# Performance work log

Measured on AMD Instinct MI355X. Metric: run time of the kernel, lower is better.

## Reference

```python
import jax, jax.numpy as jnp
import numpy as np

B, N, D = 32, 4096, 256
H, DH, S = 8, 64, 16
DI = H * DH          # dim_inner = 512
HID = 1024           # max(dim, hidden_dim)
ITERS = 3
EPS = 1e-8
SCALE = D ** (-0.5)  # NOTE: original uses dim, not dim_head


def _ln(x, g, b):
    m = jnp.mean(x, axis=-1, keepdims=True)
    v = jnp.mean((x - m) ** 2, axis=-1, keepdims=True)
    return (x - m) * jax.lax.rsqrt(v + 1e-5) * g + b


def _lin(x, W, b):  # torch layout: W [out, in]
    return x @ W.T + b


def setup_inputs() -> dict:
    key = jax.random.key(0)
    ks = jax.random.split(key, 32)

    def p(i, shape, s=0.02):
        return jax.random.normal(ks[i], shape, dtype=jnp.float32) * s

    return {
        "x": jax.random.normal(ks[0], (B, N, D), dtype=jnp.float32),
        "slots_noise": jax.random.normal(ks[1], (B, S, D), dtype=jnp.float32),
        "slots_mu": p(2, (1, 1, D), 1.0),
        "slots_logsigma": p(3, (1, 1, D)),
        "ln_in_g": jnp.ones((D,), jnp.float32), "ln_in_b": jnp.zeros((D,), jnp.float32),
        "ln_s_g": jnp.ones((D,), jnp.float32), "ln_s_b": jnp.zeros((D,), jnp.float32),
        "ln_ff_g": jnp.ones((D,), jnp.float32), "ln_ff_b": jnp.zeros((D,), jnp.float32),
        "Wq": p(4, (DI, D)), "bq": jnp.zeros((DI,), jnp.float32),
        "Wk": p(5, (DI, D)), "bk": jnp.zeros((DI,), jnp.float32),
        "Wv": p(6, (DI, D)), "bv": jnp.zeros((DI,), jnp.float32),
        "Wc": p(7, (D, DI)), "bc": jnp.zeros((D,), jnp.float32),
        "gru_wih": p(8, (3 * D, D)), "gru_whh": p(9, (3 * D, D)),
        "gru_bih": jnp.zeros((3 * D,), jnp.float32), "gru_bhh": jnp.zeros((3 * D,), jnp.float32),
        "W1": p(10, (HID, D)), "b1": jnp.zeros((HID,), jnp.float32),
        "W2": p(11, (D, HID)), "b2": jnp.zeros((D,), jnp.float32),
    }


def reference(x, slots_noise, slots_mu, slots_logsigma,
              ln_in_g, ln_in_b, ln_s_g, ln_s_b, ln_ff_g, ln_ff_b,
              Wq, bq, Wk, bk, Wv, bv, Wc, bc,
              gru_wih, gru_whh, gru_bih, gru_bhh,
              W1, b1, W2, b2):
    slots = slots_mu + jnp.exp(slots_logsigma) * slots_noise  # [B,S,D]
    xn = _ln(x, ln_in_g, ln_in_b)
    k = _lin(xn, Wk, bk).reshape(B, N, H, DH)  # [B,N,H,DH]
    v = _lin(xn, Wv, bv).reshape(B, N, H, DH)

    for _ in range(ITERS):
        slots_prev = slots
        sn = _ln(slots, ln_s_g, ln_s_b)
        q = _lin(sn, Wq, bq).reshape(B, S, H, DH)             # [B,S,H,DH]
        logits = jnp.einsum('bihd,bjhd->bhij', q, k) * SCALE  # [B,H,S,N]
        attn = jax.nn.softmax(logits, axis=-1) + EPS
        attn = attn / jnp.sum(attn, axis=-1, keepdims=True)
        upd = jnp.einsum('bhij,bjhd->bihd', attn, v).reshape(B, S, DI)
        upd = _lin(upd, Wc, bc)                               # [B,S,D]
        # GRUCell (torch gate order r, z, n)
        gi = _lin(upd.reshape(-1, D), gru_wih, gru_bih)
        gh = _lin(slots_prev.reshape(-1, D), gru_whh, gru_bhh)
        ir, iz, inn = jnp.split(gi, 3, axis=-1)
        hr, hz, hn = jnp.split(gh, 3, axis=-1)
        r = jax.nn.sigmoid(ir + hr)
        z = jax.nn.sigmoid(iz + hz)
        n = jnp.tanh(inn + r * hn)
        slots = ((1.0 - z) * n + z * slots_prev.reshape(-1, D)).reshape(B, S, D)
        slots = slots + _lin(jax.nn.relu(_lin(_ln(slots, ln_ff_g, ln_ff_b), W1, b1)), W2, b2)
    return slots
```

## Files before the change

### kernel.cpp

```cpp
#include <hip/hip_runtime.h>
#include <stdint.h>

#define B_   32
#define N_   4096
#define D_   256
#define H_   8
#define S_   16
#define DI_  512
#define HID_ 1024
#define CH_  8
#define NCHUNK_ 512
#define SCALE_ 0.0625f

typedef short  short8 __attribute__((ext_vector_type(8)));
typedef float  f32x4  __attribute__((ext_vector_type(4)));

__device__ __forceinline__ unsigned short f2bf(float x){
  union { float f; unsigned u; } v; v.f = x;
  unsigned r = v.u + 0x7FFFu + ((v.u >> 16) & 1u);
  return (unsigned short)(r >> 16);
}

#define FMA4(acc, a, Wm) do { (acc)[0] += (a)*(Wm).x; (acc)[1] += (a)*(Wm).y; (acc)[2] += (a)*(Wm).z; (acc)[3] += (a)*(Wm).w; } while(0)

__global__ void k_badws(float* out){ out[blockIdx.x*256 + threadIdx.x] = 1e9f; }

__global__ __launch_bounds__(256) void k_init_slots(
    const float* __restrict__ noise, const float* __restrict__ mu,
    const float* __restrict__ lsig, float* __restrict__ slots)
{
  int i = blockIdx.x*256 + threadIdx.x;
  int d = i & 255;
  slots[i] = mu[d] + expf(lsig[d]) * noise[i];
}

__global__ __launch_bounds__(256) void k_transpose(
    const float* __restrict__ src, float* __restrict__ dst, int R, int C)
{
  __shared__ float t[32][33];
  int c0 = blockIdx.x*32, r0 = blockIdx.y*32;
  int tx = threadIdx.x, ty = threadIdx.y;
  for (int j = 0; j < 32; j += 8){
    int r = r0 + ty + j, c = c0 + tx;
    if (r < R && c < C) t[ty+j][tx] = src[(size_t)r*C + c];
  }
  __syncthreads();
  for (int j = 0; j < 32; j += 8){
    int c = c0 + ty + j, r = r0 + tx;
    if (c < C && r < R) dst[(size_t)c*R + r] = t[tx][ty+j];
  }
}

__global__ __launch_bounds__(256) void k_ln_x(
    const float* __restrict__ x, const float* __restrict__ g, const float* __restrict__ bb,
    unsigned short* __restrict__ xn, unsigned short* __restrict__ xnT)
{
  __shared__ __align__(16) char tile[32768];
  const int blk = blockIdx.x;
  const int b  = blk >> 6;
  const int n0 = (blk & 63) * 64;
  const int t = threadIdx.x;
  const int lane = t & 63;
  const int w = t >> 6;
  float4 gv = *(const float4*)&g[lane*4];
  float4 bv = *(const float4*)&bb[lane*4];
#pragma unroll 1
  for (int it = 0; it < 16; ++it){
    const int nl = w*16 + it;
    const size_t row = (size_t)b*N_ + n0 + nl;
    float4 xv = *(const float4*)&x[row*256 + lane*4];
    float s = xv.x + xv.y + xv.z + xv.w;
    float q = xv.x*xv.x + xv.y*xv.y + xv.z*xv.z + xv.w*xv.w;
#pragma unroll
    for (int m = 1; m < 64; m <<= 1){ s += __shfl_xor(s, m); q += __shfl_xor(q, m); }
    float mean = s * 0.00390625f;
    float var  = q * 0.00390625f - mean*mean;
    float rs = rsqrtf(var + 1e-5f);
    unsigned short u0 = f2bf((xv.x-mean)*rs*gv.x + bv.x);
    unsigned short u1 = f2bf((xv.y-mean)*rs*gv.y + bv.y);
    unsigned short u2 = f2bf((xv.z-mean)*rs*gv.z + bv.z);
    unsigned short u3 = f2bf((xv.w-mean)*rs*gv.w + bv.w);
    uint2 pk; pk.x = (unsigned)u0 | ((unsigned)u1 << 16); pk.y = (unsigned)u2 | ((unsigned)u3 << 16);
    *(uint2*)&xn[row*256 + lane*4] = pk;
    *(uint2*)(tile + nl*512 + ((lane*8) ^ ((nl & 7) << 4))) = pk;
  }
  __syncthreads();
#pragma unroll 1
  for (int j = 0; j < 32; ++j){
    int flat = j*256 + t;
    int d  = flat >> 5;
    int np = (flat & 31) * 2;
    unsigned short lo = *(const unsigned short*)(tile + np*512     + ((2*d) ^ ((np     & 7) << 4)));
    unsigned short hi = *(const unsigned short*)(tile + (np+1)*512 + ((2*d) ^ (((np+1) & 7) << 4)));
    *(unsigned*)&xnT[((size_t)b*D_ + d)*N_ + n0 + np] = (unsigned)lo | ((unsigned)hi << 16);
  }
}

__global__ __launch_bounds__(256) void k_preA(
    const float* __restrict__ slots, const float* __restrict__ lsg, const float* __restrict__ lsb,
    const float* __restrict__ WqT, const float* __restrict__ bq, float* __restrict__ ql)
{
  __shared__ __align__(16) float a[4][256];
  const int lane = threadIdx.x & 63, w = threadIdx.x >> 6;
  const int row = blockIdx.x*4 + w;
  const int o   = blockIdx.y*64 + lane;
  float4 v = *(const float4*)&slots[(size_t)row*D_ + lane*4];
  float s = v.x + v.y + v.z + v.w;
  float q = v.x*v.x + v.y*v.y + v.z*v.z + v.w*v.w;
#pragma unroll
  for (int m = 1; m < 64; m <<= 1){ s += __shfl_xor(s, m); q += __shfl_xor(q, m); }
  float mean = s * 0.00390625f;
  float var  = q * 0.00390625f - mean*mean;
  float rs = rsqrtf(var + 1e-5f);
  float4 gv = *(const float4*)&lsg[lane*4];
  float4 bv = *(const float4*)&lsb[lane*4];
  a[w][lane*4+0] = (v.x-mean)*rs*gv.x + bv.x;
  a[w][lane*4+1] = (v.y-mean)*rs*gv.y + bv.y;
  a[w][lane*4+2] = (v.z-mean)*rs*gv.z + bv.z;
  a[w][lane*4+3] = (v.w-mean)*rs*gv.w + bv.w;
  const float* Wp = WqT + o;
  float acc = 0.f;
#pragma unroll 4
  for (int k4 = 0; k4 < 64; ++k4){
    float4 av = *(const float4*)&a[w][k4*4];
    acc += av.x * Wp[(size_t)(k4*4+0)*512];
    acc += av.y * Wp[(size_t)(k4*4+1)*512];
    acc += av.z * Wp[(size_t)(k4*4+2)*512];
    acc += av.w * Wp[(size_t)(k4*4+3)*512];
  }
  ql[(size_t)row*DI_ + o] = acc + bq[o];
}

__global__ __launch_bounds__(256) void k_preB(
    const float* __restrict__ ql, const float* __restrict__ Wk, const float* __restrict__ bk,
    unsigned short* __restrict__ qp, float* __restrict__ qb)
{
  __shared__ __align__(16) float qs[16][64];
  const int id = blockIdx.x;
  const int b  = id >> 3;
  const int h  = id & 7;
  const int cb = blockIdx.y;
  const int c0 = cb*64;
  const int t = threadIdx.x;
  const int lane = t & 63, w = t >> 6;
  {
    int flat = t*4;
    int s = flat >> 6, k = flat & 63;
    *(float4*)&qs[s][k] = *(const float4*)&ql[((size_t)(b*S_ + s))*DI_ + h*64 + k];
  }
  __syncthreads();
  if (cb == 0){
    float bkv = bk[h*64 + lane];
#pragma unroll
    for (int r = 0; r < 4; ++r){
      int s = w*4 + r;
      float v = qs[s][lane] * bkv;
#pragma unroll
      for (int m = 1; m < 64; m <<= 1) v += __shfl_xor(v, m);
      if (lane == 0) qb[((size_t)b*H_ + h)*S_ + s] = v * SCALE_;
    }
  }
  float acc[4] = {};
  const float* Wp = Wk + (size_t)(h*64)*256 + c0 + lane;
#pragma unroll 4
  for (int k = 0; k < 64; ++k){
    float wv = Wp[(size_t)k*256];
    acc[0] += qs[w*4+0][k] * wv;
    acc[1] += qs[w*4+1][k] * wv;
    acc[2] += qs[w*4+2][k] * wv;
    acc[3] += qs[w*4+3][k] * wv;
  }
#pragma unroll
  for (int r = 0; r < 4; ++r){
    int s = w*4 + r;
    qp[(((size_t)b*H_ + h)*S_ + s)*D_ + c0 + lane] = f2bf(SCALE_ * acc[r]);
  }
}

__global__ __launch_bounds__(512, 2) void k_flash(
    const unsigned short* __restrict__ xn, const unsigned short* __restrict__ xnT,
    const unsigned short* __restrict__ qp, const float* __restrict__ qb,
    float* __restrict__ mPart, float* __restrict__ lPart, float* __restrict__ axPart)
{
  __shared__ __align__(16) char lds[81920];
  const int ch = blockIdx.x;
  const int b  = blockIdx.y;
  const int t  = threadIdx.x;
  const int lane = t & 63;
  const int w  = t >> 6;
  const int g  = lane >> 4;
  const int c  = lane & 15;
  const int n0 = ch * NCHUNK_;

  short8 aq[8];
#pragma unroll
  for (int ks = 0; ks < 8; ++ks)
    aq[ks] = *(const short8*)&qp[(((size_t)b*H_ + w)*S_ + c)*D_ + ks*32 + g*8];
  float qbr[4];
#pragma unroll
  for (int r = 0; r < 4; ++r)
    qbr[r] = qb[((size_t)b*H_ + w)*S_ + g*4 + r];

  f32x4 accX[16];
#pragma unroll
  for (int i = 0; i < 16; ++i){ f32x4 z = {0.f,0.f,0.f,0.f}; accX[i] = z; }
  float mrun[4] = {-1e30f,-1e30f,-1e30f,-1e30f};
  float lrun[4] = {0.f,0.f,0.f,0.f};

  uint4 stA[4], stB[4];
  auto LOAD = [&](int tl){
#pragma unroll
    for (int j = 0; j < 4; ++j){
      int flat = j*64 + lane;
      int rl = w*8 + (flat >> 5);
      int gc = flat & 31;
      stA[j] = *(const uint4*)&xn[((size_t)b*N_ + n0 + tl*64 + rl)*D_ + gc*8];
      int dl = w*32 + (flat >> 3);
      int gc2 = flat & 7;
      stB[j] = *(const uint4*)&xnT[((size_t)b*D_ + dl)*N_ + n0 + tl*64 + gc2*8];
    }
  };
  auto WRITE = [&](){
#pragma unroll
    for (int j = 0; j < 4; ++j){
      int flat = j*64 + lane;
      int rl = w*8 + (flat >> 5);
      int gc = flat & 31;
      *(uint4*)(lds + rl*512 + ((gc*16) ^ ((rl & 7) << 4))) = stA[j];
      int dl = w*32 + (flat >> 3);
      int gc2 = flat & 7;
      *(uint4*)(lds + 32768 + dl*128 + ((gc2*16) ^ ((dl & 7) << 4))) = stB[j];
    }
  };

  LOAD(0); WRITE();
#pragma unroll 1
  for (int tl = 0; tl < 8; ++tl){
    __syncthreads();
    if (tl < 7) LOAD(tl + 1);
    const char* xb  = lds;
    const char* xbT = lds + 32768;
    char* pbuf = lds + 65536 + w*2048;
    f32x4 lg[4];
#pragma unroll
    for (int nf = 0; nf < 4; ++nf){ f32x4 z = {0.f,0.f,0.f,0.f}; lg[nf] = z; }
#pragma unroll
    for (int ks = 0; ks < 8; ++ks){
#pragma unroll
      for (int nf = 0; nf < 4; ++nf){
        int n = nf*16 + c;
        short8 bf = *(const short8*)(xb + n*512 + (((ks*32 + g*8)*2) ^ ((n & 7) << 4)));
        lg[nf] = __builtin_amdgcn_mfma_f32_16x16x32_bf16(aq[ks], bf, lg[nf], 0, 0, 0);
      }
    }
    float tmax[4];
#pragma unroll
    for (int r = 0; r < 4; ++r){
      lg[0][r] += qbr[r]; lg[1][r] += qbr[r]; lg[2][r] += qbr[r]; lg[3][r] += qbr[r];
      tmax[r] = fmaxf(fmaxf(lg[0][r], lg[1][r]), fmaxf(lg[2][r], lg[3][r]));
      tmax[r] = fmaxf(tmax[r], __shfl_xor(tmax[r], 1));
      tmax[r] = fmaxf(tmax[r], __shfl_xor(tmax[r], 2));
      tmax[r] = fmaxf(tmax[r], __shfl_xor(tmax[r], 4));
      tmax[r] = fmaxf(tmax[r], __shfl_xor(tmax[r], 8));
    }
    float fac[4], psum[4];
#pragma unroll
    for (int r = 0; r < 4; ++r){
      float mnew = fmaxf(mrun[r], tmax[r]);
      fac[r] = __expf(mrun[r] - mnew);
      mrun[r] = mnew;
      lrun[r] *= fac[r];
      psum[r] = 0.f;
    }
#pragma unroll
    for (int i = 0; i < 16; ++i){
      accX[i][0] *= fac[0]; accX[i][1] *= fac[1]; accX[i][2] *= fac[2]; accX[i][3] *= fac[3];
    }
#pragma unroll
    for (int nf = 0; nf < 4; ++nf){
#pragma unroll
      for (int r = 0; r < 4; ++r){
        float p = __expf(lg[nf][r] - mrun[r]);
        psum[r] += p;
        int row = g*4 + r;
        *(unsigned short*)(pbuf + row*128 + (((nf*16 + c)*2) ^ ((row & 7) << 4))) = f2bf(p);
      }
    }
#pragma unroll
    for (int r = 0; r < 4; ++r){
      psum[r] += __shfl_xor(psum[r], 1);
      psum[r] += __shfl_xor(psum[r], 2);
      psum[r] += __shfl_xor(psum[r], 4);
      psum[r] += __shfl_xor(psum[r], 8);
      lrun[r] += psum[r];
    }
#pragma unroll
    for (int ks = 0; ks < 2; ++ks){
      short8 pa = *(const short8*)(pbuf + c*128 + (((ks*32 + g*8)*2) ^ ((c & 7) << 4)));
#pragma unroll
      for (int df = 0; df < 16; ++df){
        int d = df*16 + c;
        short8 bt = *(const short8*)(xbT + d*128 + (((ks*32 + g*8)*2) ^ ((d & 7) << 4)));
        accX[df] = __builtin_amdgcn_mfma_f32_16x16x32_bf16(pa, bt, accX[df], 0, 0, 0);
      }
    }
    __syncthreads();
    if (tl < 7) WRITE();
  }
  size_t base = (((size_t)b*CH_ + ch)*H_ + w)*S_;
  if (c == 0){
#pragma unroll
    for (int r = 0; r < 4; ++r){
      mPart[base + g*4 + r] = mrun[r];
      lPart[base + g*4 + r] = lrun[r];
    }
  }
  size_t base3 = base * D_;
#pragma unroll
  for (int df = 0; df < 16; ++df){
#pragma unroll
    for (int r = 0; r < 4; ++r){
      axPart[base3 + df*256 + r*64 + lane] = accX[df][r];
    }
  }
}

__global__ __launch_bounds__(256) void k_combine(
    const float* __restrict__ mPart, const float* __restrict__ lPart, const float* __restrict__ axPart,
    const float* __restrict__ WvT, const float* __restrict__ bv, float* __restrict__ upd)
{
  __shared__ __align__(16) float av[4][256];
  const int id = blockIdx.x;
  const int b  = id >> 5;
  const int h  = (id >> 2) & 7;
  const int sq = id & 3;
  const int t = threadIdx.x;
  const int sl = t >> 6;
  const int lane = t & 63;
  const int s = sq*4 + sl;
  const int sg = s >> 2, sr = s & 3;
  const size_t pb = (((size_t)b*CH_)*H_ + h)*S_ + s;
  float mg = -1e30f;
  float mv[8], lv[8];
#pragma unroll
  for (int k = 0; k < 8; ++k){
    mv[k] = mPart[pb + (size_t)k*128];
    lv[k] = lPart[pb + (size_t)k*128];
    mg = fmaxf(mg, mv[k]);
  }
  const size_t off_s = (size_t)sr*64 + sg*16 + (lane>>2)*256 + (lane&3)*4;
  float L = 0.f, ax0 = 0.f, ax1 = 0.f, ax2 = 0.f, ax3 = 0.f;
#pragma unroll
  for (int k = 0; k < 8; ++k){
    float wgt = __expf(mv[k] - mg);
    L += lv[k]*wgt;
    size_t base3 = ((((size_t)b*CH_ + k)*H_ + h)*S_) * D_;
    float4 a4 = *(const float4*)&axPart[base3 + off_s];
    ax0 += a4.x*wgt; ax1 += a4.y*wgt; ax2 += a4.z*wgt; ax3 += a4.w*wgt;
  }
  float inv = 1.f / L;
  av[sl][lane*4+0] = ax0*inv; av[sl][lane*4+1] = ax1*inv;
  av[sl][lane*4+2] = ax2*inv; av[sl][lane*4+3] = ax3*inv;
  __syncthreads();
  float acc = bv[h*64 + lane];
  for (int d = 0; d < 256; d += 2){
    float2 a2 = *(const float2*)&av[sl][d];
    acc += a2.x * WvT[(size_t)d*512     + h*64 + lane];
    acc += a2.y * WvT[(size_t)(d+1)*512 + h*64 + lane];
  }
  upd[((size_t)b*S_ + s)*DI_ + h*64 + lane] = acc;
}

__global__ __launch_bounds__(256) void k_sA(
    const float* __restrict__ upd, const float* __restrict__ WcT,
    const float* __restrict__ bc, float* __restrict__ updc)
{
  __shared__ __align__(16) float act[4][512];
  const int lane = threadIdx.x & 63, w = threadIdx.x >> 6;
  const int row = blockIdx.x*4 + w;
  const int col = blockIdx.y*64 + lane;
  *(float4*)&act[w][lane*8]     = *(const float4*)&upd[(size_t)row*DI_ + lane*8];
  *(float4*)&act[w][lane*8 + 4] = *(const float4*)&upd[(size_t)row*DI_ + lane*8 + 4];
  const float* Wp = WcT + col;
  float acc = 0.f;
#pragma unroll 4
  for (int k4 = 0; k4 < 128; ++k4){
    float4 a = *(const float4*)&act[w][k4*4];
    acc += a.x * Wp[(size_t)(k4*4+0)*256];
    acc += a.y * Wp[(size_t)(k4*4+1)*256];
    acc += a.z * Wp[(size_t)(k4*4+2)*256];
    acc += a.w * Wp[(size_t)(k4*4+3)*256];
  }
  updc[(size_t)row*D_ + col] = acc + bc[col];
}

__global__ __launch_bounds__(256) void k_sB(
    const float* __restrict__ updc, const float* __restrict__ slots,
    const float* __restrict__ wihT, const float* __restrict__ whhT,
    const float* __restrict__ bih, const float* __restrict__ bhh,
    float* __restrict__ snl)
{
  __shared__ __align__(16) float au[4][256];
  __shared__ __align__(16) float as[4][256];
  const int lane = threadIdx.x & 63, w = threadIdx.x >> 6;
  const int row = blockIdx.x*4 + w;
  const int d   = blockIdx.y*64 + lane;
  *(float4*)&au[w][lane*4] = *(const float4*)&updc[(size_t)row*D_ + lane*4];
  *(float4*)&as[w][lane*4] = *(const float4*)&slots[(size_t)row*D_ + lane*4];
  const float* Wi = wihT + d;
  const float* Wh = whhT + d;
  float air=0.f, aiz=0.f, ain=0.f, ahr=0.f, ahz=0.f, ahn=0.f;
#pragma unroll 2
  for (int k4 = 0; k4 < 64; ++k4){
    float4 u = *(const float4*)&au[w][k4*4];
    float4 s = *(const float4*)&as[w][k4*4];
#pragma unroll
    for (int j = 0; j < 4; ++j){
      int k = k4*4 + j;
      float uv = (j==0)?u.x:(j==1)?u.y:(j==2)?u.z:u.w;
      float sv = (j==0)?s.x:(j==1)?s.y:(j==2)?s.z:s.w;
      air += uv * Wi[(size_t)k*768];
      aiz += uv * Wi[(size_t)k*768 + 256];
      ain += uv * Wi[(size_t)k*768 + 512];
      ahr += sv * Wh[(size_t)k*768];
      ahz += sv * Wh[(size_t)k*768 + 256];
      ahn += sv * Wh[(size_t)k*768 + 512];
    }
  }
  float ir = air + bih[d]     + ahr + bhh[d];
  float iz = aiz + bih[256+d] + ahz + bhh[256+d];
  float rg = 1.f/(1.f + __expf(-ir));
  float zg = 1.f/(1.f + __expf(-iz));
  float ng = tanhf(ain + bih[512+d] + rg*(ahn + bhh[512+d]));
  snl[(size_t)row*D_ + d] = (1.f - zg)*ng + zg*as[w][d];
}

__global__ __launch_bounds__(256) void k_sC(
    const float* __restrict__ snl, const float* __restrict__ lfg, const float* __restrict__ lfb,
    const float* __restrict__ W1T, const float* __restrict__ b1, float* __restrict__ h1)
{
  __shared__ __align__(16) float a[4][256];
  const int lane = threadIdx.x & 63, w = threadIdx.x >> 6;
  const int row = blockIdx.x*4 + w;
  const int o   = blockIdx.y*64 + lane;
  float4 v = *(const float4*)&snl[(size_t)row*D_ + lane*4];
  float s = v.x + v.y + v.z + v.w;
  float q = v.x*v.x + v.y*v.y + v.z*v.z + v.w*v.w;
#pragma unroll
  for (int m = 1; m < 64; m <<= 1){ s += __shfl_xor(s, m); q += __shfl_xor(q, m); }
  float mean = s * 0.00390625f;
  float var  = q * 0.00390625f - mean*mean;
  float rs = rsqrtf(var + 1e-5f);
  float4 gv = *(const float4*)&lfg[lane*4];
  float4 bv = *(const float4*)&lfb[lane*4];
  a[w][lane*4+0] = (v.x-mean)*rs*gv.x + bv.x;
  a[w][lane*4+1] = (v.y-mean)*rs*gv.y + bv.y;
  a[w][lane*4+2] = (v.z-mean)*rs*gv.z + bv.z;
  a[w][lane*4+3] = (v.w-mean)*rs*gv.w + bv.w;
  const float* Wp = W1T + o;
  float acc = 0.f;
#pragma unroll 4
  for (int k4 = 0; k4 < 64; ++k4){
    float4 av = *(const float4*)&a[w][k4*4];
    acc += av.x * Wp[(size_t)(k4*4+0)*1024];
    acc += av.y * Wp[(size_t)(k4*4+1)*1024];
    acc += av.z * Wp[(size_t)(k4*4+2)*1024];
    acc += av.w * Wp[(size_t)(k4*4+3)*1024];
  }
  h1[(size_t)row*HID_ + o] = fmaxf(acc + b1[o], 0.f);
}

__global__ __launch_bounds__(256) void k_sD(
    const float* __restrict__ h1, const float* __restrict__ snl,
    const float* __restrict__ W2T, const float* __restrict__ b2, float* __restrict__ dst)
{
  __shared__ __align__(16) float a[4][1024];
  const int lane = threadIdx.x & 63, w = threadIdx.x >> 6;
  const int row = blockIdx.x*4 + w;
  const int o   = blockIdx.y*64 + lane;
#pragma unroll
  for (int j = 0; j < 4; ++j)
    *(float4*)&a[w][lane*16 + j*4] = *(const float4*)&h1[(size_t)row*HID_ + lane*16 + j*4];
  const float* Wp = W2T + o;
  float acc = 0.f;
#pragma unroll 4
  for (int k4 = 0; k4 < 256; ++k4){
    float4 av = *(const float4*)&a[w][k4*4];
    acc += av.x * Wp[(size_t)(k4*4+0)*256];
    acc += av.y * Wp[(size_t)(k4*4+1)*256];
    acc += av.z * Wp[(size_t)(k4*4+2)*256];
    acc += av.w * Wp[(size_t)(k4*4+3)*256];
  }
  dst[(size_t)row*D_ + o] = snl[(size_t)row*D_ + o] + acc + b2[o];
}

extern "C" void kernel_launch(void* const* d_in, const int* in_sizes, int n_in,
                              void* d_out, int out_size, void* d_ws, size_t ws_size,
                              hipStream_t stream)
{
  const float* x       = (const float*)d_in[0];
  const float* noise   = (const float*)d_in[1];
  const float* mu      = (const float*)d_in[2];
  const float* lsig    = (const float*)d_in[3];
  const float* ln_in_g = (const float*)d_in[4];
  const float* ln_in_b = (const float*)d_in[5];
  const float* ln_s_g  = (const float*)d_in[6];
  const float* ln_s_b  = (const float*)d_in[7];
  const float* ln_ff_g = (const float*)d_in[8];
  const float* ln_ff_b = (const float*)d_in[9];
  const float* Wq  = (const float*)d_in[10]; const float* bq  = (const float*)d_in[11];
  const float* Wk  = (const float*)d_in[12]; const float* bk  = (const float*)d_in[13];
  const float* Wv  = (const float*)d_in[14]; const float* bv  = (const float*)d_in[15];
  const float* Wc  = (const float*)d_in[16]; const float* bc  = (const float*)d_in[17];
  const float* wih = (const float*)d_in[18]; const float* whh = (const float*)d_in[19];
  const float* bih = (const float*)d_in[20]; const float* bhh = (const float*)d_in[21];
  const float* W1  = (const float*)d_in[22]; const float* b1  = (const float*)d_in[23];
  const float* W2  = (const float*)d_in[24]; const float* b2  = (const float*)d_in[25];

  char* ws = (char*)d_ws;
  unsigned short* xn  = (unsigned short*)(ws + 0);
  unsigned short* xnT = (unsigned short*)(ws + 67108864);
  float* slots = (float*)(ws + 134217728);
  unsigned short* qp = (unsigned short*)(ws + 134742016);
  float* qb   = (float*)(ws + 136839168);
  float* mP   = (float*)(ws + 136855552);
  float* lP   = (float*)(ws + 136986624);
  float* axP  = (float*)(ws + 137117696);
  float* upd  = (float*)(ws + 170672128);
  float* WqT  = (float*)(ws + 171720704);
  float* WvT  = (float*)(ws + 172244992);
  float* WcT  = (float*)(ws + 172769280);
  float* wihT = (float*)(ws + 173293568);
  float* whhT = (float*)(ws + 174080000);
  float* W1T  = (float*)(ws + 174866432);
  float* W2T  = (float*)(ws + 175915008);
  float* updc = (float*)(ws + 137117696);
  float* snl  = (float*)(ws + 137641984);
  float* h1   = (float*)(ws + 138166272);
  float* ql   = (float*)(ws + 141000704);

  if (ws_size < (size_t)176963584ull){
    k_badws<<<512, 256, 0, stream>>>((float*)d_out);
    return;
  }

  k_init_slots<<<512, 256, 0, stream>>>(noise, mu, lsig, slots);
  k_ln_x<<<2048, 256, 0, stream>>>(x, ln_in_g, ln_in_b, xn, xnT);
  dim3 tb(32, 8);
  k_transpose<<<dim3(8, 16), tb, 0, stream>>>(Wq,  WqT,  512,  256);
  k_transpose<<<dim3(8, 16), tb, 0, stream>>>(Wv,  WvT,  512,  256);
  k_transpose<<<dim3(16, 8), tb, 0, stream>>>(Wc,  WcT,  256,  512);
  k_transpose<<<dim3(8, 24), tb, 0, stream>>>(wih, wihT, 768,  256);
  k_transpose<<<dim3(8, 24), tb, 0, stream>>>(whh, whhT, 768,  256);
  k_transpose<<<dim3(8, 32), tb, 0, stream>>>(W1,  W1T,  1024, 256);
  k_transpose<<<dim3(32, 8), tb, 0, stream>>>(W2,  W2T,  256,  1024);

  for (int it = 0; it < 3; ++it){
    k_preA<<<dim3(128, 8), 256, 0, stream>>>(slots, ln_s_g, ln_s_b, WqT, bq, ql);
    k_preB<<<dim3(256, 4), 256, 0, stream>>>(ql, Wk, bk, qp, qb);
    k_flash<<<dim3(CH_, B_), 512, 0, stream>>>(xn, xnT, qp, qb, mP, lP, axP);
    k_combine<<<1024, 256, 0, stream>>>(mP, lP, axP, WvT, bv, upd);
    k_sA<<<dim3(128, 4),  256, 0, stream>>>(upd, WcT, bc, updc);
    k_sB<<<dim3(128, 4),  256, 0, stream>>>(updc, slots, wihT, whhT, bih, bhh, snl);
    k_sC<<<dim3(128, 16), 256, 0, stream>>>(snl, ln_ff_g, ln_ff_b, W1T, b1, h1);
    k_sD<<<dim3(128, 4),  256, 0, stream>>>(h1, snl, W2T, b2, (it == 2) ? (float*)d_out : slots);
  }
}
```

Baseline: 684.3 us.

## Double-buffer flash tiles with direct global-to-LDS loads

Replaces the register-staged copy of the xn and xnT tiles into shared memory with `global_load_lds` instructions that write straight into a second LDS buffer. The swizzle moves from the LDS write address to the global read address. The next tile is loaded while the current one is computed, which removes the staging registers and the separate write phase. Shared memory grows to about 144KB, so two blocks can no longer fit per CU. The grid is only 256 blocks, so this may not matter, but correctness depends on the barrier waiting for the async LDS loads to finish.

```diff
diff --git a/kernel.cpp b/kernel.cpp
--- a/kernel.cpp
+++ b/kernel.cpp
@@ -19,6 +19,12 @@
   union { float f; unsigned u; } v; v.f = x;
   unsigned r = v.u + 0x7FFFu + ((v.u >> 16) & 1u);
   return (unsigned short)(r >> 16);
+}
+
+__device__ __forceinline__ void gld16(const void* g, void* l){
+  __builtin_amdgcn_global_load_lds(
+      (const __attribute__((address_space(1))) unsigned int*)g,
+      (__attribute__((address_space(3))) unsigned int*)l, 16, 0, 0);
 }
 
 #define FMA4(acc, a, Wm) do { (acc)[0] += (a)*(Wm).x; (acc)[1] += (a)*(Wm).y; (acc)[2] += (a)*(Wm).z; (acc)[3] += (a)*(Wm).w; } while(0)
@@ -182,7 +188,7 @@
     const unsigned short* __restrict__ qp, const float* __restrict__ qb,
     float* __restrict__ mPart, float* __restrict__ lPart, float* __restrict__ axPart)
 {
-  __shared__ __align__(16) char lds[81920];
+  __shared__ __align__(16) char lds[147456];
   const int ch = blockIdx.x;
   const int b  = blockIdx.y;
   const int t  = threadIdx.x;
@@ -207,40 +213,33 @@
   float mrun[4] = {-1e30f,-1e30f,-1e30f,-1e30f};
   float lrun[4] = {0.f,0.f,0.f,0.f};
 
-  uint4 stA[4], stB[4];
-  auto LOAD = [&](int tl){
+  auto ISSUE = [&](int tl, int buf){
+    char* lb = lds + buf*65536;
 #pragma unroll
     for (int j = 0; j < 4; ++j){
-      int flat = j*64 + lane;
-      int rl = w*8 + (flat >> 5);
-      int gc = flat & 31;
-      stA[j] = *(const uint4*)&xn[((size_t)b*N_ + n0 + tl*64 + rl)*D_ + gc*8];
-      int dl = w*32 + (flat >> 3);
-      int gc2 = flat & 7;
-      stB[j] = *(const uint4*)&xnT[((size_t)b*D_ + dl)*N_ + n0 + tl*64 + gc2*8];
+      int rl = w*8 + j*2 + (lane >> 5);
+      int cs = (lane & 31) ^ (rl & 7);
+      gld16(&xn[((size_t)b*N_ + n0 + tl*64 + rl)*D_ + cs*8],
+            lb + (w*8 + j*2)*512);
+    }
+#pragma unroll
+    for (int j = 0; j < 4; ++j){
+      int dl = w*32 + j*8 + (lane >> 3);
+      int cs = (lane & 7) ^ (dl & 7);
+      gld16(&xnT[((size_t)b*D_ + dl)*N_ + n0 + tl*64 + cs*8],
+            lb + 32768 + (w*32 + j*8)*128);
     }
   };
-  auto WRITE = [&](){
-#pragma unroll
-    for (int j = 0; j < 4; ++j){
-      int flat = j*64 + lane;
-      int rl = w*8 + (flat >> 5);
-      int gc = flat & 31;
-      *(uint4*)(lds + rl*512 + ((gc*16) ^ ((rl & 7) << 4))) = stA[j];
-      int dl = w*32 + (flat >> 3);
-      int gc2 = flat & 7;
-      *(uint4*)(lds + 32768 + dl*128 + ((gc2*16) ^ ((dl & 7) << 4))) = stB[j];
-    }
-  };
-
-  LOAD(0); WRITE();
+
+  ISSUE(0, 0);
+  __syncthreads();
+  int cur = 0;
 #pragma unroll 1
   for (int tl = 0; tl < 8; ++tl){
-    __syncthreads();
-    if (tl < 7) LOAD(tl + 1);
-    const char* xb  = lds;
-    const char* xbT = lds + 32768;
-    char* pbuf = lds + 65536 + w*2048;
+    if (tl < 7) ISSUE(tl + 1, cur ^ 1);
+    const char* xb  = lds + cur*65536;
+    const char* xbT = lds + cur*65536 + 32768;
+    char* pbuf = lds + 131072 + w*2048;
     f32x4 lg[4];
 #pragma unroll
     for (int nf = 0; nf < 4; ++nf){ f32x4 z = {0.f,0.f,0.f,0.f}; lg[nf] = z; }
@@ -305,7 +304,7 @@
       }
     }
     __syncthreads();
-    if (tl < 7) WRITE();
+    cur ^= 1;
   }
   size_t base = (((size_t)b*CH_ + ch)*H_ + w)*S_;
   if (c == 0){
```

New measurement: 577.6 us. -15.6%, faster.
